# Kernel optimization log

Measured on AMD Instinct MI355X. Metric: run time of the kernel, lower is better.

Reference implementation:

```python
import jax, jax.numpy as jnp
import numpy as np

SEQ, BATCH = 128, 256
INPUT_BITS, STATE_BITS = 256, 256
N_IN, N_ST = 1024, 256        # n_state_neurons == state_size_bits (recurrence constraint)
NB_IN, NB_ST = 16, 16         # bits per neuron -> RAM size 2**16 per neuron


def setup_inputs() -> dict:
    key = jax.random.key(0)
    k1, k2, k3, k4, k5, k6 = jax.random.split(key, 6)
    input_seq_bits = jax.random.randint(k1, (SEQ, BATCH, INPUT_BITS), 0, 2).astype(bool)
    init_state = jax.random.randint(k2, (BATCH, STATE_BITS), 0, 2).astype(bool)
    # random bit connections: input layer reads from input_bits+state_bits (512),
    # state layer reads from input_layer_out+state_bits (1280)
    input_conn = jax.random.randint(k3, (N_IN, NB_IN), 0, INPUT_BITS + STATE_BITS)
    state_conn = jax.random.randint(k5, (N_ST, NB_ST), 0, N_IN + STATE_BITS)
    # per-neuron RAM contents (bool words)
    input_mem = jax.random.randint(k4, (N_IN, 2 ** NB_IN), 0, 2).astype(bool)
    state_mem = jax.random.randint(k6, (N_ST, 2 ** NB_ST), 0, 2).astype(bool)
    return {
        "input_seq_bits": input_seq_bits,
        "init_state": init_state,
        "input_conn": input_conn,
        "input_mem": input_mem,
        "state_conn": state_conn,
        "state_mem": state_mem,
    }


def _ram(bits, conn, mem):
    # bits: [B, T_bits] bool; conn: [N, nb] int; mem: [N, 2**nb]
    sel = bits[:, conn].astype(jnp.int32)                 # [B, N, nb]
    w = (1 << jnp.arange(conn.shape[1], dtype=jnp.int32))  # bit k -> 2**k
    addr = jnp.sum(sel * w, axis=-1)                      # [B, N]
    return mem[jnp.arange(mem.shape[0])[None, :], addr]   # [B, N]


def reference(input_seq_bits, init_state, input_conn, input_mem, state_conn, state_mem):
    def step(state, inp):
        # input_layer: [input_bits | prev_state]
        io = _ram(jnp.concatenate([inp, state], axis=1), input_conn, input_mem)
        # state_layer: [input_layer_out | prev_state]
        ns = _ram(jnp.concatenate([io, state], axis=1), state_conn, state_mem)
        return ns, io

    final_state, outs = jax.lax.scan(step, init_state, input_seq_bits)
    return outs, final_state  # [SEQ, BATCH, N_IN] bool, [BATCH, N_ST] bool
```

## Files before the change

### kernel.cpp

```cpp
#include <hip/hip_runtime.h>
#include <stdint.h>

#define SEQ 128
#define BATCH 256
#define INPUT_BITS 256
#define STATE_BITS 256
#define N_IN 1024
#define N_ST 256
#define NB 16
#define RAM_WORDS 2048

__global__ void pack_bits_kernel(const uint32_t* __restrict__ src,
                                 uint32_t* __restrict__ dst) {
    int i = blockIdx.x * blockDim.x + threadIdx.x;
    uint32_t v = src[i];
    uint64_t m = __ballot(v != 0u);
    int lane = threadIdx.x & 63;
    if ((lane & 31) == 0) {
        dst[i >> 5] = (uint32_t)(m >> (lane & 32));
    }
}

__global__ __launch_bounds__(1024)
void ram_automaton_kernel(
    const uint32_t* __restrict__ seq_bits,
    const uint32_t* __restrict__ init_state,
    const int*      __restrict__ input_conn,
    const int*      __restrict__ state_conn,
    const uint32_t* __restrict__ pim,
    const uint32_t* __restrict__ psm,
    const uint32_t* __restrict__ im_raw,
    const uint32_t* __restrict__ sm_raw,
    int* __restrict__ outs,
    int* __restrict__ final_state,
    int packed)
{
    __shared__ uint32_t c0[16];
    __shared__ uint32_t c1[40];

    const int b = blockIdx.x;
    const int tid = threadIdx.x;
    const int lane = tid & 63;

    int ic[NB];
#pragma unroll
    for (int k = 0; k < NB; k++) ic[k] = input_conn[tid * NB + k];
    int sc[NB];
    if (tid < N_ST) {
#pragma unroll
        for (int k = 0; k < NB; k++) sc[k] = state_conn[tid * NB + k];
    }

    if (tid < STATE_BITS) {
        uint32_t v = init_state[(size_t)b * STATE_BITS + tid];
        uint64_t m = __ballot(v != 0u);
        if ((lane & 31) == 0) {
            uint32_t w = (uint32_t)(m >> (lane & 32));
            c0[8 + (tid >> 5)] = w;
            c1[32 + (tid >> 5)] = w;
        }
    }
    __syncthreads();

    for (int t = 0; t < SEQ; t++) {
        if (tid < INPUT_BITS) {
            uint32_t v = seq_bits[((size_t)t * BATCH + b) * INPUT_BITS + tid];
            uint64_t m = __ballot(v != 0u);
            if ((lane & 31) == 0) c0[tid >> 5] = (uint32_t)(m >> (lane & 32));
        }
        __syncthreads();

        {
            int addr = 0;
#pragma unroll
            for (int k = 0; k < NB; k++) {
                int c = ic[k];
                uint32_t w = c0[c >> 5];
                addr |= (int)((w >> (c & 31)) & 1u) << k;
            }
            uint32_t bit;
            if (packed) {
                uint32_t w = pim[(tid << 11) + (addr >> 5)];
                bit = (w >> (addr & 31)) & 1u;
            } else {
                bit = (im_raw[((size_t)tid << 16) + (size_t)addr] != 0u) ? 1u : 0u;
            }
            outs[((size_t)t * BATCH + b) * N_IN + tid] = (int)bit;
            uint64_t m = __ballot(bit != 0u);
            if (lane == 0) {
                c1[(tid >> 5)]     = (uint32_t)m;
                c1[(tid >> 5) + 1] = (uint32_t)(m >> 32);
            }
        }
        __syncthreads();

        uint32_t nsbit = 0;
        if (tid < N_ST) {
            int addr = 0;
#pragma unroll
            for (int k = 0; k < NB; k++) {
                int c = sc[k];
                uint32_t w = c1[c >> 5];
                addr |= (int)((w >> (c & 31)) & 1u) << k;
            }
            if (packed) {
                uint32_t w = psm[(tid << 11) + (addr >> 5)];
                nsbit = (w >> (addr & 31)) & 1u;
            } else {
                nsbit = (sm_raw[((size_t)tid << 16) + (size_t)addr] != 0u) ? 1u : 0u;
            }
        }
        __syncthreads();

        if (tid < N_ST) {
            uint64_t m = __ballot(nsbit != 0u);
            if ((lane & 31) == 0) {
                uint32_t w = (uint32_t)(m >> (lane & 32));
                c0[8 + (tid >> 5)]  = w;
                c1[32 + (tid >> 5)] = w;
            }
        }
        __syncthreads();
    }

    if (tid < N_ST) {
        uint32_t w = c0[8 + (tid >> 5)];
        final_state[(size_t)b * N_ST + tid] = (int)((w >> (tid & 31)) & 1u);
    }
}

extern "C" void kernel_launch(void* const* d_in, const int* in_sizes, int n_in,
                              void* d_out, int out_size, void* d_ws, size_t ws_size,
                              hipStream_t stream) {
    const uint32_t* seq        = (const uint32_t*)d_in[0];
    const uint32_t* init_state = (const uint32_t*)d_in[1];
    const int*      input_conn = (const int*)d_in[2];
    const uint32_t* input_mem  = (const uint32_t*)d_in[3];
    const int*      state_conn = (const int*)d_in[4];
    const uint32_t* state_mem  = (const uint32_t*)d_in[5];

    int* outs = (int*)d_out;
    int* fin  = outs + (size_t)SEQ * BATCH * N_IN;

    const size_t pim_words = (size_t)N_IN * RAM_WORDS;
    const size_t psm_words = (size_t)N_ST * RAM_WORDS;
    const size_t need = (pim_words + psm_words) * sizeof(uint32_t);

    uint32_t* pim = nullptr;
    uint32_t* psm = nullptr;
    int packed = 0;
    if (ws_size >= need) {
        packed = 1;
        pim = (uint32_t*)d_ws;
        psm = pim + pim_words;
        hipLaunchKernelGGL(pack_bits_kernel,
                           dim3((N_IN * 65536) / 256), dim3(256), 0, stream,
                           input_mem, pim);
        hipLaunchKernelGGL(pack_bits_kernel,
                           dim3((N_ST * 65536) / 256), dim3(256), 0, stream,
                           state_mem, psm);
    }

    hipLaunchKernelGGL(ram_automaton_kernel, dim3(BATCH), dim3(1024), 0, stream,
                       seq, init_state, input_conn, state_conn,
                       pim, psm, input_mem, state_mem, outs, fin, packed);
}
```

Measured before the change: 986.2 us.

## Vectorize RAM bit packing and prefetch inputs, dropping a barrier per step

The pack kernel now has each thread read 32 words with 128-bit nontemporal loads and build one packed word, where before one ballot per 32 elements was used. This aims to make the full-size RAM conversion, which dominates the traffic, bandwidth-efficient. In the main kernel the next step's input bit is prefetched into a register and the state ballot is merged into the step-start ballot, removing one __syncthreads per timestep. Output stores become nontemporal. The state update now relies on keeping nsbit in registers across iterations.

```diff
diff --git a/kernel.cpp b/kernel.cpp
--- a/kernel.cpp
+++ b/kernel.cpp
@@ -10,15 +10,22 @@
 #define NB 16
 #define RAM_WORDS 2048
 
-__global__ void pack_bits_kernel(const uint32_t* __restrict__ src,
-                                 uint32_t* __restrict__ dst) {
+typedef uint32_t u32x4 __attribute__((ext_vector_type(4)));
+
+__global__ __launch_bounds__(256)
+void pack_bits_kernel(const u32x4* __restrict__ src, uint32_t* __restrict__ dst) {
     int i = blockIdx.x * blockDim.x + threadIdx.x;
-    uint32_t v = src[i];
-    uint64_t m = __ballot(v != 0u);
-    int lane = threadIdx.x & 63;
-    if ((lane & 31) == 0) {
-        dst[i >> 5] = (uint32_t)(m >> (lane & 32));
+    const u32x4* p = src + (size_t)i * 8;
+    uint32_t w = 0;
+#pragma unroll
+    for (int j = 0; j < 8; j++) {
+        u32x4 v = __builtin_nontemporal_load(p + j);
+        w |= (v.x != 0u ? 1u : 0u) << (4 * j + 0);
+        w |= (v.y != 0u ? 1u : 0u) << (4 * j + 1);
+        w |= (v.z != 0u ? 1u : 0u) << (4 * j + 2);
+        w |= (v.w != 0u ? 1u : 0u) << (4 * j + 3);
     }
+    dst[i] = w;
 }
 
 __global__ __launch_bounds__(1024)
@@ -51,24 +58,29 @@
         for (int k = 0; k < NB; k++) sc[k] = state_conn[tid * NB + k];
     }
 
-    if (tid < STATE_BITS) {
-        uint32_t v = init_state[(size_t)b * STATE_BITS + tid];
-        uint64_t m = __ballot(v != 0u);
-        if ((lane & 31) == 0) {
-            uint32_t w = (uint32_t)(m >> (lane & 32));
-            c0[8 + (tid >> 5)] = w;
-            c1[32 + (tid >> 5)] = w;
-        }
-    }
-    __syncthreads();
+    uint32_t nsbit = 0;
+    if (tid < N_ST) nsbit = (init_state[(size_t)b * STATE_BITS + tid] != 0u) ? 1u : 0u;
+
+    uint32_t inbit = 0;
+    if (tid < INPUT_BITS) inbit = seq_bits[((size_t)0 * BATCH + b) * INPUT_BITS + tid];
 
     for (int t = 0; t < SEQ; t++) {
         if (tid < INPUT_BITS) {
-            uint32_t v = seq_bits[((size_t)t * BATCH + b) * INPUT_BITS + tid];
-            uint64_t m = __ballot(v != 0u);
-            if ((lane & 31) == 0) c0[tid >> 5] = (uint32_t)(m >> (lane & 32));
+            uint64_t mi = __ballot(inbit != 0u);
+            uint64_t ms = __ballot(nsbit != 0u);
+            if ((lane & 31) == 0) {
+                c0[tid >> 5] = (uint32_t)(mi >> (lane & 32));
+                uint32_t ws = (uint32_t)(ms >> (lane & 32));
+                c0[8 + (tid >> 5)]  = ws;
+                c1[32 + (tid >> 5)] = ws;
+            }
         }
         __syncthreads();
+
+        if (t + 1 < SEQ && tid < INPUT_BITS) {
+            inbit = __builtin_nontemporal_load(
+                seq_bits + ((size_t)(t + 1) * BATCH + b) * INPUT_BITS + tid);
+        }
 
         {
             int addr = 0;
@@ -85,7 +97,8 @@
             } else {
                 bit = (im_raw[((size_t)tid << 16) + (size_t)addr] != 0u) ? 1u : 0u;
             }
-            outs[((size_t)t * BATCH + b) * N_IN + tid] = (int)bit;
+            __builtin_nontemporal_store((int)bit,
+                outs + ((size_t)t * BATCH + b) * N_IN + tid);
             uint64_t m = __ballot(bit != 0u);
             if (lane == 0) {
                 c1[(tid >> 5)]     = (uint32_t)m;
@@ -94,7 +107,6 @@
         }
         __syncthreads();
 
-        uint32_t nsbit = 0;
         if (tid < N_ST) {
             int addr = 0;
 #pragma unroll
@@ -111,21 +123,10 @@
             }
         }
         __syncthreads();
-
-        if (tid < N_ST) {
-            uint64_t m = __ballot(nsbit != 0u);
-            if ((lane & 31) == 0) {
-                uint32_t w = (uint32_t)(m >> (lane & 32));
-                c0[8 + (tid >> 5)]  = w;
-                c1[32 + (tid >> 5)] = w;
-            }
-        }
-        __syncthreads();
     }
 
     if (tid < N_ST) {
-        uint32_t w = c0[8 + (tid >> 5)];
-        final_state[(size_t)b * N_ST + tid] = (int)((w >> (tid & 31)) & 1u);
+        final_state[(size_t)b * N_ST + tid] = (int)nsbit;
     }
 }
 
@@ -154,11 +155,11 @@
         pim = (uint32_t*)d_ws;
         psm = pim + pim_words;
         hipLaunchKernelGGL(pack_bits_kernel,
-                           dim3((N_IN * 65536) / 256), dim3(256), 0, stream,
-                           input_mem, pim);
+                           dim3((unsigned)(pim_words / 256)), dim3(256), 0, stream,
+                           (const u32x4*)input_mem, pim);
         hipLaunchKernelGGL(pack_bits_kernel,
-                           dim3((N_ST * 65536) / 256), dim3(256), 0, stream,
-                           state_mem, psm);
+                           dim3((unsigned)(psm_words / 256)), dim3(256), 0, stream,
+                           (const u32x4*)state_mem, psm);
     }
 
     hipLaunchKernelGGL(ram_automaton_kernel, dim3(BATCH), dim3(1024), 0, stream,
```

After: 946.1 us. 1.04x faster.
